# Kernel optimization log

Hardware: AMD Instinct MI355X
Metric: run time of the kernel (lower is better)

## Reference

```python
import jax, jax.numpy as jnp
import numpy as np

N_NODES = 50000
N_EDGES = 800000
IN_CH, HID_CH, OUT_CH = 256, 128, 64


def setup_inputs() -> dict:
    key = jax.random.key(0)
    k_x, k_e, k_w1, k_w2 = jax.random.split(key, 4)
    x = jax.random.normal(k_x, (N_NODES, IN_CH), dtype=jnp.float32)
    edge_index = jax.random.randint(k_e, (2, N_EDGES), 0, N_NODES, dtype=jnp.int32)
    # Glorot-style init like PyG GCNConv (weight [in, out], bias zeros)
    s1 = float(np.sqrt(6.0 / (IN_CH + HID_CH)))
    s2 = float(np.sqrt(6.0 / (HID_CH + OUT_CH)))
    W1 = jax.random.uniform(k_w1, (IN_CH, HID_CH), jnp.float32, -s1, s1)
    b1 = jnp.zeros((HID_CH,), jnp.float32)
    W2 = jax.random.uniform(k_w2, (HID_CH, OUT_CH), jnp.float32, -s2, s2)
    b2 = jnp.zeros((OUT_CH,), jnp.float32)
    return {"x": x, "edge_index": edge_index, "W1": W1, "b1": b1, "W2": W2, "b2": b2}


def _gcn_conv(x, src, dst, deg_inv_sqrt, W, b, n_nodes):
    """GCNConv with self-loops: D^{-1/2}(A+I)D^{-1/2} X W + b."""
    h = x @ W  # [N, out]
    norm = deg_inv_sqrt[src] * deg_inv_sqrt[dst]          # [E]
    msgs = h[src] * norm[:, None]                          # [E, out] gather
    agg = jax.ops.segment_sum(msgs, dst, num_segments=n_nodes)  # scatter-add
    self_loop = h * (deg_inv_sqrt * deg_inv_sqrt)[:, None]      # self-loop term
    return agg + self_loop + b


def reference(x, edge_index, W1, b1, W2, b2):
    n = x.shape[0]
    src, dst = edge_index[0], edge_index[1]
    # degree includes self-loop (+1), edge weight 1, counted at destination
    deg = jnp.zeros((n,), x.dtype).at[dst].add(1.0) + 1.0
    dis = jax.lax.rsqrt(deg)
    h = jax.nn.relu(_gcn_conv(x, src, dst, dis, W1, b1, n))
    out = jax.nn.relu(_gcn_conv(h, src, dst, dis, W2, b2, n))
    return out
```

## Files before the change

kernel.cpp:

```cpp
#include <hip/hip_runtime.h>

#define N_NODES 50000
#define N_EDGES 800000
#define IN_CH 256
#define HID_CH 128
#define OUT_CH 64
#define CAP 64
#define NBINS 196
#define PCHUNK 3200
#define PBLOCKS 250
#define SWZ_BLOCKS ((IN_CH * HID_CH + HID_CH * OUT_CH) / 256)

typedef _Float16 f16;
typedef _Float16 f16x8 __attribute__((ext_vector_type(8)));
typedef _Float16 f16x2 __attribute__((ext_vector_type(2)));
typedef float f32x4 __attribute__((ext_vector_type(4)));
typedef unsigned short u16;
typedef unsigned int u32;

__device__ __forceinline__ void local_scan(const int* __restrict__ binCnt,
                                           int* sc ,
                                           int* vout ) {
    int t = threadIdx.x & 255;
    int v = t < NBINS ? binCnt[t] : 0;
    sc[t] = v;
    vout[t] = v;
    __syncthreads();
#pragma unroll
    for (int ofs = 1; ofs < 256; ofs <<= 1) {
        int add = (t >= ofs) ? sc[t - ofs] : 0;
        __syncthreads();
        sc[t] += add;
        __syncthreads();
    }
}

template <int K, int N>
__device__ __forceinline__ void swz(const float* __restrict__ W, f16* __restrict__ Bsw,
                                    int idx) {
    constexpr int NTILES = N / 16;
    int j = idx & 7;
    int lane = (idx >> 3) & 63;
    int rest = idx >> 9;
    int nt = rest % NTILES;
    int ks = rest / NTILES;
    int k = ks * 32 + (lane >> 4) * 8 + j;
    int n = nt * 16 + (lane & 15);
    Bsw[idx] = (f16)W[(size_t)k * N + n];
}

__global__ __launch_bounds__(256) void k_pre(const int* __restrict__ dst,
                                             int* __restrict__ binCnt, int E,
                                             const float* __restrict__ W1,
                                             const float* __restrict__ W2,
                                             f16* __restrict__ B1,
                                             f16* __restrict__ B2) {
    if ((int)blockIdx.x < PBLOCKS) {
        __shared__ int lcnt[NBINS];
        for (int i = threadIdx.x; i < NBINS; i += 256) lcnt[i] = 0;
        __syncthreads();
        int base = blockIdx.x * PCHUNK;
        int end = min(base + PCHUNK, E);
        for (int i = base + (int)threadIdx.x; i < end; i += 256)
            atomicAdd(&lcnt[dst[i] >> 8], 1);
        __syncthreads();
        for (int i = threadIdx.x; i < NBINS; i += 256)
            if (lcnt[i]) atomicAdd(&binCnt[i], lcnt[i]);
        return;
    }
    int idx = ((int)blockIdx.x - PBLOCKS) * 256 + threadIdx.x;
    if (idx < IN_CH * HID_CH) {
        swz<IN_CH, HID_CH>(W1, B1, idx);
    } else {
        idx -= IN_CH * HID_CH;
        if (idx < HID_CH * OUT_CH) swz<HID_CH, OUT_CH>(W2, B2, idx);
    }
}

__global__ __launch_bounds__(256) void k_place(const int* __restrict__ src,
                                               const int* __restrict__ dst,
                                               const int* __restrict__ binCnt,
                                               int* __restrict__ binCursor,
                                               u32* __restrict__ ebuf, int E) {
    __shared__ u32 codes[PCHUNK];
    __shared__ int sc[256], vv[256];
    __shared__ int lcnt[NBINS], lbase[NBINS], lcur[NBINS];
    local_scan(binCnt, sc, vv);
    for (int i = threadIdx.x; i < NBINS; i += 256) lcnt[i] = 0;
    __syncthreads();
    int base = blockIdx.x * PCHUNK;
    int m = min(PCHUNK, E - base);
    for (int j = threadIdx.x; j < m; j += 256) {
        u32 d = (u32)dst[base + j];
        codes[j] = (d << 16) | (u32)src[base + j];
        atomicAdd(&lcnt[d >> 8], 1);
    }
    __syncthreads();
    for (int i = threadIdx.x; i < NBINS; i += 256) {
        lbase[i] = (sc[i] - vv[i]) + atomicAdd(&binCursor[i], lcnt[i]);
        lcur[i] = 0;
    }
    __syncthreads();
    for (int j = threadIdx.x; j < m; j += 256) {
        u32 c = codes[j];
        int b = c >> 24;
        int p = atomicAdd(&lcur[b], 1);
        ebuf[lbase[b] + p] = c;
    }
}

__global__ __launch_bounds__(256) void k_build(const u32* __restrict__ ebuf,
                                               const int* __restrict__ binCnt,
                                               int* __restrict__ cnt,
                                               float* __restrict__ dis,
                                               u16* __restrict__ bucket, int N) {
    __shared__ int sc[256], vv[256];
    __shared__ int lcnt[256];
    __shared__ u16 lbuck[256 * CAP];
    local_scan(binCnt, sc, vv);
    int t = threadIdx.x;
    lcnt[t] = 0;
    __syncthreads();
    int b = blockIdx.x;
    int s = sc[b] - vv[b];
    int e = sc[b];
    for (int i = s + t; i < e; i += 256) {
        u32 c = ebuf[i];
        int local = (c >> 16) & 255;
        int p = atomicAdd(&lcnt[local], 1);
        if (p < CAP) lbuck[local * CAP + p] = (u16)(c & 0xFFFFu);
    }
    __syncthreads();
    int nodeBase = b << 8;
    if (nodeBase + t < N) {
        cnt[nodeBase + t] = lcnt[t];
        dis[nodeBase + t] = rsqrtf((float)lcnt[t] + 1.0f);
    }
    const uint4* lsrc = (const uint4*)lbuck;
    uint4* gdst = (uint4*)(bucket + (size_t)nodeBase * CAP);
    for (int idx = t; idx < 256 * CAP / 8; idx += 256) {
        int row = idx >> 3;
        if (nodeBase + row < N) gdst[idx] = lsrc[idx];
    }
}

template <int K, int N, bool A_FP32, bool RELU>
__global__ __launch_bounds__(256) void k_gemm(const void* __restrict__ Av,
                                              const f16* __restrict__ Bsw,
                                              const float* __restrict__ dis,
                                              f16* __restrict__ C, int M) {
    constexpr int KSTEPS = K / 32, NTILES = N / 16;
    const int tid = threadIdx.x;
    const int wave = tid >> 6, lane = tid & 63;
    const int quad = lane >> 4, l16 = lane & 15;
    int row = blockIdx.x * 64 + wave * 16 + l16;
    const int rowc = row < M ? row : M - 1;

    f32x4 acc[NTILES];
#pragma unroll
    for (int t = 0; t < NTILES; ++t) acc[t] = (f32x4){0.f, 0.f, 0.f, 0.f};

#pragma unroll
    for (int ks = 0; ks < KSTEPS; ++ks) {
        f16x8 afrag;
        if (A_FP32) {
            const float* A = (const float*)Av;
            const float4* p = (const float4*)(A + (size_t)rowc * K + ks * 32 + quad * 8);
            float4 v0 = p[0], v1 = p[1];
            afrag[0] = (f16)v0.x; afrag[1] = (f16)v0.y;
            afrag[2] = (f16)v0.z; afrag[3] = (f16)v0.w;
            afrag[4] = (f16)v1.x; afrag[5] = (f16)v1.y;
            afrag[6] = (f16)v1.z; afrag[7] = (f16)v1.w;
        } else {
            const f16* A = (const f16*)Av;
            afrag = *(const f16x8*)(A + (size_t)rowc * K + ks * 32 + quad * 8);
            if (RELU) {
#pragma unroll
                for (int j = 0; j < 8; ++j)
                    afrag[j] = afrag[j] > (f16)0 ? afrag[j] : (f16)0;
            }
        }
#pragma unroll
        for (int t = 0; t < NTILES; ++t) {
            f16x8 bfrag = *(const f16x8*)(Bsw + (((size_t)ks * NTILES + t) * 64 + lane) * 8);
            acc[t] = __builtin_amdgcn_mfma_f32_16x16x32_f16(afrag, bfrag, acc[t], 0, 0, 0);
        }
    }

    int rbase = blockIdx.x * 64 + wave * 16 + quad * 4;
#pragma unroll
    for (int r = 0; r < 4; ++r) {
        int gr = rbase + r;
        if (gr < M) {
            float d = dis[gr];
#pragma unroll
            for (int t = 0; t < NTILES; ++t)
                C[(size_t)gr * N + t * 16 + l16] = (f16)(acc[t][r] * d);
        }
    }
}

#define APAD 136
__global__ __launch_bounds__(512) void k_pullgemm(const f16* __restrict__ g1,
                                                  const float* __restrict__ dis,
                                                  const float* __restrict__ b1,
                                                  const int* __restrict__ cnt,
                                                  const u16* __restrict__ bucket,
                                                  const f16* __restrict__ W2sw,
                                                  f16* __restrict__ g2, int N) {
    __shared__ f16 As[64][APAD];
    const int tid = threadIdx.x;
    const int wave = tid >> 6, lane = tid & 63;
    const int base = blockIdx.x * 64;

    float bv0 = b1[lane * 2], bv1 = b1[lane * 2 + 1];
    for (int i = 0; i < 8; ++i) {
        int uloc = wave * 8 + i;
        int u = base + uloc;
        if (u >= N) {
            f16x2 z; z[0] = (f16)0; z[1] = (f16)0;
            *(f16x2*)&As[uloc][lane * 2] = z;
            continue;
        }
        const f16* gp = g1 + lane * 2;
        f16x2 hv = *(const f16x2*)(gp + (size_t)u * HID_CH);
        float a0 = (float)hv[0], a1 = (float)hv[1];

        int n = cnt[u];
        if (n > CAP) n = CAP;
        const u16* row = bucket + u * CAP;
        int k = 0;
        for (; k + 8 <= n; k += 8) {
            uint4 iv = *(const uint4*)(row + k);
            int s0 = iv.x & 0xFFFF, s1 = iv.x >> 16;
            int s2 = iv.y & 0xFFFF, s3 = iv.y >> 16;
            int s4 = iv.z & 0xFFFF, s5 = iv.z >> 16;
            int s6 = iv.w & 0xFFFF, s7 = iv.w >> 16;
            f16x2 v0 = *(const f16x2*)(gp + (size_t)s0 * HID_CH);
            f16x2 v1 = *(const f16x2*)(gp + (size_t)s1 * HID_CH);
            f16x2 v2 = *(const f16x2*)(gp + (size_t)s2 * HID_CH);
            f16x2 v3 = *(const f16x2*)(gp + (size_t)s3 * HID_CH);
            f16x2 v4 = *(const f16x2*)(gp + (size_t)s4 * HID_CH);
            f16x2 v5 = *(const f16x2*)(gp + (size_t)s5 * HID_CH);
            f16x2 v6 = *(const f16x2*)(gp + (size_t)s6 * HID_CH);
            f16x2 v7 = *(const f16x2*)(gp + (size_t)s7 * HID_CH);
            a0 += ((float)v0[0] + (float)v1[0]) + ((float)v2[0] + (float)v3[0]) +
                  (((float)v4[0] + (float)v5[0]) + ((float)v6[0] + (float)v7[0]));
            a1 += ((float)v0[1] + (float)v1[1]) + ((float)v2[1] + (float)v3[1]) +
                  (((float)v4[1] + (float)v5[1]) + ((float)v6[1] + (float)v7[1]));
        }
        if (k + 4 <= n) {
            ushort4 s4v = *(const ushort4*)(row + k);
            f16x2 v0 = *(const f16x2*)(gp + (size_t)s4v.x * HID_CH);
            f16x2 v1 = *(const f16x2*)(gp + (size_t)s4v.y * HID_CH);
            f16x2 v2 = *(const f16x2*)(gp + (size_t)s4v.z * HID_CH);
            f16x2 v3 = *(const f16x2*)(gp + (size_t)s4v.w * HID_CH);
            a0 += ((float)v0[0] + (float)v1[0]) + ((float)v2[0] + (float)v3[0]);
            a1 += ((float)v0[1] + (float)v1[1]) + ((float)v2[1] + (float)v3[1]);
            k += 4;
        }
        for (; k < n; ++k) {
            f16x2 v = *(const f16x2*)(gp + (size_t)row[k] * HID_CH);
            a0 += (float)v[0];
            a1 += (float)v[1];
        }

        float du = dis[u];
        f16x2 o;
        o[0] = (f16)fmaxf(fmaf(du, a0, bv0), 0.f);
        o[1] = (f16)fmaxf(fmaf(du, a1, bv1), 0.f);
        *(f16x2*)&As[uloc][lane * 2] = o;
    }
    __syncthreads();

    constexpr int KSTEPS = HID_CH / 32;
    const int rg = wave >> 1;
    const int half = wave & 1;
    const int quad = lane >> 4, l16 = lane & 15;

    f32x4 acc[2];
    acc[0] = (f32x4){0.f, 0.f, 0.f, 0.f};
    acc[1] = (f32x4){0.f, 0.f, 0.f, 0.f};

#pragma unroll
    for (int ks = 0; ks < KSTEPS; ++ks) {
        f16x8 afrag = *(const f16x8*)&As[rg * 16 + l16][ks * 32 + quad * 8];
#pragma unroll
        for (int tt = 0; tt < 2; ++tt) {
            int nt = half * 2 + tt;
            f16x8 bfrag = *(const f16x8*)(W2sw + (((size_t)ks * 4 + nt) * 64 + lane) * 8);
            acc[tt] = __builtin_amdgcn_mfma_f32_16x16x32_f16(afrag, bfrag, acc[tt], 0, 0, 0);
        }
    }

    int rbase = base + rg * 16 + quad * 4;
#pragma unroll
    for (int r = 0; r < 4; ++r) {
        int gr = rbase + r;
        if (gr < N) {
            float d = dis[gr];
#pragma unroll
            for (int tt = 0; tt < 2; ++tt) {
                int nt = half * 2 + tt;
                g2[(size_t)gr * OUT_CH + nt * 16 + l16] = (f16)(acc[tt][r] * d);
            }
        }
    }
}

__global__ __launch_bounds__(256) void k_pull2(const f16* __restrict__ g,
                                               const float* __restrict__ dis,
                                               const float* __restrict__ bias,
                                               const int* __restrict__ cnt,
                                               const u16* __restrict__ bucket,
                                               float2* __restrict__ out, int N) {
    int tid = blockIdx.x * 256 + threadIdx.x;
    int u = tid >> 5;
    int sub = tid & 31;
    if (u >= N) return;
    const f16* gp = g + sub * 2;

    f16x2 hv = *(const f16x2*)(gp + (size_t)u * OUT_CH);
    float a0 = (float)hv[0], a1 = (float)hv[1];

    int n = cnt[u];
    if (n > CAP) n = CAP;
    const u16* row = bucket + u * CAP;

    int k = 0;
    for (; k + 8 <= n; k += 8) {
        uint4 iv = *(const uint4*)(row + k);
        int s0 = iv.x & 0xFFFF, s1 = iv.x >> 16;
        int s2 = iv.y & 0xFFFF, s3 = iv.y >> 16;
        int s4 = iv.z & 0xFFFF, s5 = iv.z >> 16;
        int s6 = iv.w & 0xFFFF, s7 = iv.w >> 16;
        f16x2 v0 = *(const f16x2*)(gp + (size_t)s0 * OUT_CH);
        f16x2 v1 = *(const f16x2*)(gp + (size_t)s1 * OUT_CH);
        f16x2 v2 = *(const f16x2*)(gp + (size_t)s2 * OUT_CH);
        f16x2 v3 = *(const f16x2*)(gp + (size_t)s3 * OUT_CH);
        f16x2 v4 = *(const f16x2*)(gp + (size_t)s4 * OUT_CH);
        f16x2 v5 = *(const f16x2*)(gp + (size_t)s5 * OUT_CH);
        f16x2 v6 = *(const f16x2*)(gp + (size_t)s6 * OUT_CH);
        f16x2 v7 = *(const f16x2*)(gp + (size_t)s7 * OUT_CH);
        a0 += ((float)v0[0] + (float)v1[0]) + ((float)v2[0] + (float)v3[0]) +
              (((float)v4[0] + (float)v5[0]) + ((float)v6[0] + (float)v7[0]));
        a1 += ((float)v0[1] + (float)v1[1]) + ((float)v2[1] + (float)v3[1]) +
              (((float)v4[1] + (float)v5[1]) + ((float)v6[1] + (float)v7[1]));
    }
    if (k + 4 <= n) {
        ushort4 s4v = *(const ushort4*)(row + k);
        f16x2 v0 = *(const f16x2*)(gp + (size_t)s4v.x * OUT_CH);
        f16x2 v1 = *(const f16x2*)(gp + (size_t)s4v.y * OUT_CH);
        f16x2 v2 = *(const f16x2*)(gp + (size_t)s4v.z * OUT_CH);
        f16x2 v3 = *(const f16x2*)(gp + (size_t)s4v.w * OUT_CH);
        a0 += ((float)v0[0] + (float)v1[0]) + ((float)v2[0] + (float)v3[0]);
        a1 += ((float)v0[1] + (float)v1[1]) + ((float)v2[1] + (float)v3[1]);
        k += 4;
    }
    for (; k < n; ++k) {
        f16x2 v = *(const f16x2*)(gp + (size_t)row[k] * OUT_CH);
        a0 += (float)v[0];
        a1 += (float)v[1];
    }

    float du = dis[u];
    float o0 = fmaf(du, a0, bias[sub * 2]);
    float o1 = fmaf(du, a1, bias[sub * 2 + 1]);
    out[(size_t)u * 32 + sub] = make_float2(fmaxf(o0, 0.f), fmaxf(o1, 0.f));
}


extern "C" void kernel_launch(void* const* d_in, const int* in_sizes, int n_in,
                              void* d_out, int out_size, void* d_ws, size_t ws_size,
                              hipStream_t stream) {
    const float* x  = (const float*)d_in[0];
    const int* ei   = (const int*)d_in[1];
    const float* W1 = (const float*)d_in[2];
    const float* b1 = (const float*)d_in[3];
    const float* W2 = (const float*)d_in[4];
    const float* b2 = (const float*)d_in[5];
    float* out = (float*)d_out;

    const int* src = ei;
    const int* dst = ei + N_EDGES;

    char* ws = (char*)d_ws;
    size_t off = 0;
    auto alloc = [&](size_t bytes) -> void* {
        off = (off + 255) & ~(size_t)255;
        void* p = ws + off;
        off += bytes;
        return p;
    };
    int*   binCnt    = (int*)alloc((size_t)NBINS * 2 * 4);
    int*   binCursor = binCnt + NBINS;
    u32*   ebuf      = (u32*)alloc((size_t)N_EDGES * 4);
    int*   cnt       = (int*)alloc((size_t)N_NODES * 4);
    float* dis       = (float*)alloc((size_t)N_NODES * 4);
    u16*   bucket    = (u16*)alloc((size_t)N_NODES * CAP * 2);
    f16*   W1sw      = (f16*)alloc((size_t)IN_CH * HID_CH * 2);
    f16*   W2sw      = (f16*)alloc((size_t)HID_CH * OUT_CH * 2);
    f16*   g1        = (f16*)alloc((size_t)N_NODES * HID_CH * 2);
    f16*   g2        = (f16*)alloc((size_t)N_NODES * OUT_CH * 2);

    hipMemsetAsync(binCnt, 0, (size_t)NBINS * 2 * 4, stream);

    k_pre<<<PBLOCKS + SWZ_BLOCKS, 256, 0, stream>>>(dst, binCnt, N_EDGES,
                                                    W1, W2, W1sw, W2sw);
    k_place<<<PBLOCKS, 256, 0, stream>>>(src, dst, binCnt, binCursor, ebuf, N_EDGES);
    k_build<<<NBINS, 256, 0, stream>>>(ebuf, binCnt, cnt, dis, bucket, N_NODES);

    k_gemm<IN_CH, HID_CH, true, false><<<(N_NODES + 63) / 64, 256, 0, stream>>>(
        x, W1sw, dis, g1, N_NODES);

    k_pullgemm<<<(N_NODES + 63) / 64, 512, 0, stream>>>(g1, dis, b1, cnt, bucket,
                                                        W2sw, g2, N_NODES);

    k_pull2<<<(N_NODES * 32 + 255) / 256, 256, 0, stream>>>(g2, dis, b2, cnt, bucket,
                                                            (float2*)out, N_NODES);
}
```

Baseline: 203.3 us.

## Fuse GCN pipeline into one cooperative persistent kernel with grid syncs

Replaces the six separate kernel launches with a single cooperative persistent kernel of 256 blocks x 512 threads. Grid-wide syncs separate the phases (histogram, place, build, gemm, pullgemm, pull2). The first GEMM no longer waits for degrees: the src-side dis scaling moves into the gather loops and is applied per neighbour, so GEMM1 can overlap with edge placement on a separate set of blocks, guarded by a flag spin-wait on the weight swizzle. The aim is to remove launch gaps and tail idle time. In exchange it adds grid-sync costs, an extra dis load per gathered edge, and lower occupancy from the fixed grid, with the old separate kernels kept as a fallback.

Result: slower. 642.9 us (+216.2%).

```diff
diff --git a/kernel.cpp b/kernel.cpp
--- a/kernel.cpp
+++ b/kernel.cpp
@@ -1,4 +1,7 @@
 #include <hip/hip_runtime.h>
+#include <hip/hip_cooperative_groups.h>
+
+namespace cg = cooperative_groups;
 
 #define N_NODES 50000
 #define N_EDGES 800000
@@ -7,33 +10,25 @@
 #define OUT_CH 64
 #define CAP 64
 #define NBINS 196
-#define PCHUNK 3200
-#define PBLOCKS 250
-#define SWZ_BLOCKS ((IN_CH * HID_CH + HID_CH * OUT_CH) / 256)
+#define NTHREADS 512
+#define NBLOCKS 256
+#define PBLOCKS 128
+#define PCHUNK 6250
+#define GB (NBLOCKS - PBLOCKS)
+#define SWZ_ELEMS (IN_CH * HID_CH + HID_CH * OUT_CH)
+#define SWZ_BLOCKS (SWZ_ELEMS / NTHREADS)
+#define G1_TILES ((N_NODES + 127) / 128)
+#define PG_TILES ((N_NODES + 63) / 64)
+#define APAD 136
 
 typedef _Float16 f16;
 typedef _Float16 f16x8 __attribute__((ext_vector_type(8)));
+typedef _Float16 f16x4v __attribute__((ext_vector_type(4)));
 typedef _Float16 f16x2 __attribute__((ext_vector_type(2)));
 typedef float f32x4 __attribute__((ext_vector_type(4)));
 typedef unsigned short u16;
 typedef unsigned int u32;
 
-__device__ __forceinline__ void local_scan(const int* __restrict__ binCnt,
-                                           int* sc ,
-                                           int* vout ) {
-    int t = threadIdx.x & 255;
-    int v = t < NBINS ? binCnt[t] : 0;
-    sc[t] = v;
-    vout[t] = v;
-    __syncthreads();
-#pragma unroll
-    for (int ofs = 1; ofs < 256; ofs <<= 1) {
-        int add = (t >= ofs) ? sc[t - ofs] : 0;
-        __syncthreads();
-        sc[t] += add;
-        __syncthreads();
-    }
-}
 
 template <int K, int N>
 __device__ __forceinline__ void swz(const float* __restrict__ W, f16* __restrict__ Bsw,
@@ -49,59 +44,65 @@
     Bsw[idx] = (f16)W[(size_t)k * N + n];
 }
 
-__global__ __launch_bounds__(256) void k_pre(const int* __restrict__ dst,
-                                             int* __restrict__ binCnt, int E,
-                                             const float* __restrict__ W1,
-                                             const float* __restrict__ W2,
-                                             f16* __restrict__ B1,
-                                             f16* __restrict__ B2) {
-    if ((int)blockIdx.x < PBLOCKS) {
-        __shared__ int lcnt[NBINS];
-        for (int i = threadIdx.x; i < NBINS; i += 256) lcnt[i] = 0;
+__device__ __forceinline__ void swz_all(int idx, const float* __restrict__ W1,
+                                        const float* __restrict__ W2,
+                                        f16* __restrict__ W1sw, f16* __restrict__ W2sw) {
+    if (idx < IN_CH * HID_CH) swz<IN_CH, HID_CH>(W1, W1sw, idx);
+    else if (idx < SWZ_ELEMS) swz<HID_CH, OUT_CH>(W2, W2sw, idx - IN_CH * HID_CH);
+}
+
+__device__ __forceinline__ void hist_chunk(int chunk, const int* __restrict__ dst,
+                                           int* __restrict__ binCnt, int* lcnt) {
+    const int tid = threadIdx.x;
+    for (int i = tid; i < NBINS; i += NTHREADS) lcnt[i] = 0;
+    __syncthreads();
+    int base = chunk * PCHUNK;
+    for (int i = tid; i < PCHUNK; i += NTHREADS)
+        atomicAdd(&lcnt[dst[base + i] >> 8], 1);
+    __syncthreads();
+    for (int i = tid; i < NBINS; i += NTHREADS)
+        if (lcnt[i]) atomicAdd(&binCnt[i], lcnt[i]);
+}
+
+__device__ __forceinline__ void scan_local(const int* __restrict__ binCnt,
+                                           int* sc, int* vv) {
+    const int t = threadIdx.x;
+    if (t < 256) {
+        int v = (t < NBINS) ? binCnt[t] : 0;
+        sc[t] = v; vv[t] = v;
+    }
+    __syncthreads();
+    for (int ofs = 1; ofs < 256; ofs <<= 1) {
+        int add = 0;
+        if (t < 256 && t >= ofs) add = sc[t - ofs];
         __syncthreads();
-        int base = blockIdx.x * PCHUNK;
-        int end = min(base + PCHUNK, E);
-        for (int i = base + (int)threadIdx.x; i < end; i += 256)
-            atomicAdd(&lcnt[dst[i] >> 8], 1);
+        if (t < 256) sc[t] += add;
         __syncthreads();
-        for (int i = threadIdx.x; i < NBINS; i += 256)
-            if (lcnt[i]) atomicAdd(&binCnt[i], lcnt[i]);
-        return;
-    }
-    int idx = ((int)blockIdx.x - PBLOCKS) * 256 + threadIdx.x;
-    if (idx < IN_CH * HID_CH) {
-        swz<IN_CH, HID_CH>(W1, B1, idx);
-    } else {
-        idx -= IN_CH * HID_CH;
-        if (idx < HID_CH * OUT_CH) swz<HID_CH, OUT_CH>(W2, B2, idx);
-    }
-}
-
-__global__ __launch_bounds__(256) void k_place(const int* __restrict__ src,
-                                               const int* __restrict__ dst,
-                                               const int* __restrict__ binCnt,
-                                               int* __restrict__ binCursor,
-                                               u32* __restrict__ ebuf, int E) {
-    __shared__ u32 codes[PCHUNK];
-    __shared__ int sc[256], vv[256];
-    __shared__ int lcnt[NBINS], lbase[NBINS], lcur[NBINS];
-    local_scan(binCnt, sc, vv);
-    for (int i = threadIdx.x; i < NBINS; i += 256) lcnt[i] = 0;
-    __syncthreads();
-    int base = blockIdx.x * PCHUNK;
-    int m = min(PCHUNK, E - base);
-    for (int j = threadIdx.x; j < m; j += 256) {
+    }
+}
+
+__device__ __forceinline__ void place_chunk(int chunk, const int* __restrict__ src,
+                                            const int* __restrict__ dst,
+                                            const int* sc, const int* vv,
+                                            int* __restrict__ binCursor,
+                                            u32* __restrict__ ebuf,
+                                            u32* codes, int* lcnt, int* lbase, int* lcur) {
+    const int tid = threadIdx.x;
+    for (int i = tid; i < NBINS; i += NTHREADS) lcnt[i] = 0;
+    __syncthreads();
+    int base = chunk * PCHUNK;
+    for (int j = tid; j < PCHUNK; j += NTHREADS) {
         u32 d = (u32)dst[base + j];
         codes[j] = (d << 16) | (u32)src[base + j];
         atomicAdd(&lcnt[d >> 8], 1);
     }
     __syncthreads();
-    for (int i = threadIdx.x; i < NBINS; i += 256) {
+    for (int i = tid; i < NBINS; i += NTHREADS) {
         lbase[i] = (sc[i] - vv[i]) + atomicAdd(&binCursor[i], lcnt[i]);
         lcur[i] = 0;
     }
     __syncthreads();
-    for (int j = threadIdx.x; j < m; j += 256) {
+    for (int j = tid; j < PCHUNK; j += NTHREADS) {
         u32 c = codes[j];
         int b = c >> 24;
         int p = atomicAdd(&lcur[b], 1);
@@ -109,22 +110,16 @@
     }
 }
 
-__global__ __launch_bounds__(256) void k_build(const u32* __restrict__ ebuf,
-                                               const int* __restrict__ binCnt,
-                                               int* __restrict__ cnt,
-                                               float* __restrict__ dis,
-                                               u16* __restrict__ bucket, int N) {
-    __shared__ int sc[256], vv[256];
-    __shared__ int lcnt[256];
-    __shared__ u16 lbuck[256 * CAP];
-    local_scan(binCnt, sc, vv);
-    int t = threadIdx.x;
-    lcnt[t] = 0;
-    __syncthreads();
-    int b = blockIdx.x;
-    int s = sc[b] - vv[b];
-    int e = sc[b];
-    for (int i = s + t; i < e; i += 256) {
+__device__ __forceinline__ void build_bin(int b, const u32* __restrict__ ebuf,
+                                          const int* sc, const int* vv,
+                                          int* __restrict__ cnt, float* __restrict__ dis,
+                                          u16* __restrict__ bucket,
+                                          int* lcnt, u16* lbuck) {
+    const int tid = threadIdx.x;
+    if (tid < 256) lcnt[tid] = 0;
+    __syncthreads();
+    int s = sc[b] - vv[b], e = sc[b];
+    for (int i = s + tid; i < e; i += NTHREADS) {
         u32 c = ebuf[i];
         int local = (c >> 16) & 255;
         int p = atomicAdd(&lcnt[local], 1);
@@ -132,99 +127,85 @@
     }
     __syncthreads();
     int nodeBase = b << 8;
-    if (nodeBase + t < N) {
-        cnt[nodeBase + t] = lcnt[t];
-        dis[nodeBase + t] = rsqrtf((float)lcnt[t] + 1.0f);
-    }
-    const uint4* lsrc = (const uint4*)lbuck;
-    uint4* gdst = (uint4*)(bucket + (size_t)nodeBase * CAP);
-    for (int idx = t; idx < 256 * CAP / 8; idx += 256) {
+    if (tid < 256 && nodeBase + tid < N_NODES) {
+        cnt[nodeBase + tid] = lcnt[tid];
+        dis[nodeBase + tid] = rsqrtf((float)lcnt[tid] + 1.0f);
+    }
+    const uint4* ls = (const uint4*)lbuck;
+    uint4* gd = (uint4*)(bucket + (size_t)nodeBase * CAP);
+    for (int idx = tid; idx < 256 * CAP / 8; idx += NTHREADS) {
         int row = idx >> 3;
-        if (nodeBase + row < N) gdst[idx] = lsrc[idx];
-    }
-}
-
-template <int K, int N, bool A_FP32, bool RELU>
-__global__ __launch_bounds__(256) void k_gemm(const void* __restrict__ Av,
-                                              const f16* __restrict__ Bsw,
-                                              const float* __restrict__ dis,
-                                              f16* __restrict__ C, int M) {
-    constexpr int KSTEPS = K / 32, NTILES = N / 16;
+        if (nodeBase + row < N_NODES) gd[idx] = ls[idx];
+    }
+}
+
+__device__ __forceinline__ void gemm1_tile(int t, const float* __restrict__ x,
+                                           const f16* __restrict__ W1sw,
+                                           f16* __restrict__ h1) {
     const int tid = threadIdx.x;
     const int wave = tid >> 6, lane = tid & 63;
     const int quad = lane >> 4, l16 = lane & 15;
-    int row = blockIdx.x * 64 + wave * 16 + l16;
-    const int rowc = row < M ? row : M - 1;
-
-    f32x4 acc[NTILES];
-#pragma unroll
-    for (int t = 0; t < NTILES; ++t) acc[t] = (f32x4){0.f, 0.f, 0.f, 0.f};
-
-#pragma unroll
-    for (int ks = 0; ks < KSTEPS; ++ks) {
+    int row = t * 128 + wave * 16 + l16;
+    const int rowc = row < N_NODES ? row : N_NODES - 1;
+
+    f32x4 acc[8];
+#pragma unroll
+    for (int n = 0; n < 8; ++n) acc[n] = (f32x4){0.f, 0.f, 0.f, 0.f};
+#pragma unroll
+    for (int ks = 0; ks < 8; ++ks) {
+        const float4* p = (const float4*)(x + (size_t)rowc * IN_CH + ks * 32 + quad * 8);
+        float4 v0 = p[0], v1 = p[1];
         f16x8 afrag;
-        if (A_FP32) {
-            const float* A = (const float*)Av;
-            const float4* p = (const float4*)(A + (size_t)rowc * K + ks * 32 + quad * 8);
-            float4 v0 = p[0], v1 = p[1];
-            afrag[0] = (f16)v0.x; afrag[1] = (f16)v0.y;
-            afrag[2] = (f16)v0.z; afrag[3] = (f16)v0.w;
-            afrag[4] = (f16)v1.x; afrag[5] = (f16)v1.y;
-            afrag[6] = (f16)v1.z; afrag[7] = (f16)v1.w;
-        } else {
-            const f16* A = (const f16*)Av;
-            afrag = *(const f16x8*)(A + (size_t)rowc * K + ks * 32 + quad * 8);
-            if (RELU) {
-#pragma unroll
-                for (int j = 0; j < 8; ++j)
-                    afrag[j] = afrag[j] > (f16)0 ? afrag[j] : (f16)0;
-            }
-        }
-#pragma unroll
-        for (int t = 0; t < NTILES; ++t) {
-            f16x8 bfrag = *(const f16x8*)(Bsw + (((size_t)ks * NTILES + t) * 64 + lane) * 8);
-            acc[t] = __builtin_amdgcn_mfma_f32_16x16x32_f16(afrag, bfrag, acc[t], 0, 0, 0);
-        }
-    }
-
-    int rbase = blockIdx.x * 64 + wave * 16 + quad * 4;
+        afrag[0] = (f16)v0.x; afrag[1] = (f16)v0.y;
+        afrag[2] = (f16)v0.z; afrag[3] = (f16)v0.w;
+        afrag[4] = (f16)v1.x; afrag[5] = (f16)v1.y;
+        afrag[6] = (f16)v1.z; afrag[7] = (f16)v1.w;
+#pragma unroll
+        for (int nt = 0; nt < 8; ++nt) {
+            f16x8 bfrag = *(const f16x8*)(W1sw + (((size_t)ks * 8 + nt) * 64 + lane) * 8);
+            acc[nt] = __builtin_amdgcn_mfma_f32_16x16x32_f16(afrag, bfrag, acc[nt], 0, 0, 0);
+        }
+    }
+    int rbase = t * 128 + wave * 16 + quad * 4;
 #pragma unroll
     for (int r = 0; r < 4; ++r) {
         int gr = rbase + r;
-        if (gr < M) {
-            float d = dis[gr];
-#pragma unroll
-            for (int t = 0; t < NTILES; ++t)
-                C[(size_t)gr * N + t * 16 + l16] = (f16)(acc[t][r] * d);
-        }
-    }
-}
-
-#define APAD 136
-__global__ __launch_bounds__(512) void k_pullgemm(const f16* __restrict__ g1,
-                                                  const float* __restrict__ dis,
-                                                  const float* __restrict__ b1,
-                                                  const int* __restrict__ cnt,
-                                                  const u16* __restrict__ bucket,
-                                                  const f16* __restrict__ W2sw,
-                                                  f16* __restrict__ g2, int N) {
-    __shared__ f16 As[64][APAD];
+        if (gr < N_NODES) {
+#pragma unroll
+            for (int nt = 0; nt < 8; ++nt)
+                h1[(size_t)gr * HID_CH + nt * 16 + l16] = (f16)acc[nt][r];
+        }
+    }
+}
+
+__device__ __forceinline__ void pullgemm_tile(int t, f16* AsRaw,
+                                              const f16* __restrict__ h1,
+                                              const float* __restrict__ dis,
+                                              const float* __restrict__ b1,
+                                              const int* __restrict__ cnt,
+                                              const u16* __restrict__ bucket,
+                                              const f16* __restrict__ W2sw,
+                                              f16* __restrict__ g2) {
+    typedef f16 (*As_t)[APAD];
+    As_t As = (As_t)AsRaw;
     const int tid = threadIdx.x;
     const int wave = tid >> 6, lane = tid & 63;
-    const int base = blockIdx.x * 64;
+    const int base = t * 64;
 
     float bv0 = b1[lane * 2], bv1 = b1[lane * 2 + 1];
     for (int i = 0; i < 8; ++i) {
         int uloc = wave * 8 + i;
         int u = base + uloc;
-        if (u >= N) {
+        if (u >= N_NODES) {
             f16x2 z; z[0] = (f16)0; z[1] = (f16)0;
             *(f16x2*)&As[uloc][lane * 2] = z;
             continue;
         }
-        const f16* gp = g1 + lane * 2;
+        float du = dis[u];
+        const f16* gp = h1 + lane * 2;
         f16x2 hv = *(const f16x2*)(gp + (size_t)u * HID_CH);
-        float a0 = (float)hv[0], a1 = (float)hv[1];
+        float a0 = du * (float)hv[0];
+        float a1 = du * (float)hv[1];
 
         int n = cnt[u];
         if (n > CAP) n = CAP;
@@ -236,6 +217,8 @@
             int s2 = iv.y & 0xFFFF, s3 = iv.y >> 16;
             int s4 = iv.z & 0xFFFF, s5 = iv.z >> 16;
             int s6 = iv.w & 0xFFFF, s7 = iv.w >> 16;
+            float d0 = dis[s0], d1 = dis[s1], d2 = dis[s2], d3 = dis[s3];
+            float d4 = dis[s4], d5 = dis[s5], d6 = dis[s6], d7 = dis[s7];
             f16x2 v0 = *(const f16x2*)(gp + (size_t)s0 * HID_CH);
             f16x2 v1 = *(const f16x2*)(gp + (size_t)s1 * HID_CH);
             f16x2 v2 = *(const f16x2*)(gp + (size_t)s2 * HID_CH);
@@ -244,28 +227,22 @@
             f16x2 v5 = *(const f16x2*)(gp + (size_t)s5 * HID_CH);
             f16x2 v6 = *(const f16x2*)(gp + (size_t)s6 * HID_CH);
             f16x2 v7 = *(const f16x2*)(gp + (size_t)s7 * HID_CH);
-            a0 += ((float)v0[0] + (float)v1[0]) + ((float)v2[0] + (float)v3[0]) +
-                  (((float)v4[0] + (float)v5[0]) + ((float)v6[0] + (float)v7[0]));
-            a1 += ((float)v0[1] + (float)v1[1]) + ((float)v2[1] + (float)v3[1]) +
-                  (((float)v4[1] + (float)v5[1]) + ((float)v6[1] + (float)v7[1]));
-        }
-        if (k + 4 <= n) {
-            ushort4 s4v = *(const ushort4*)(row + k);
-            f16x2 v0 = *(const f16x2*)(gp + (size_t)s4v.x * HID_CH);
-            f16x2 v1 = *(const f16x2*)(gp + (size_t)s4v.y * HID_CH);
-            f16x2 v2 = *(const f16x2*)(gp + (size_t)s4v.z * HID_CH);
-            f16x2 v3 = *(const f16x2*)(gp + (size_t)s4v.w * HID_CH);
-            a0 += ((float)v0[0] + (float)v1[0]) + ((float)v2[0] + (float)v3[0]);
-            a1 += ((float)v0[1] + (float)v1[1]) + ((float)v2[1] + (float)v3[1]);
-            k += 4;
+            a0 = fmaf(d0, (float)v0[0], a0); a1 = fmaf(d0, (float)v0[1], a1);
+            a0 = fmaf(d1, (float)v1[0], a0); a1 = fmaf(d1, (float)v1[1], a1);
+            a0 = fmaf(d2, (float)v2[0], a0); a1 = fmaf(d2, (float)v2[1], a1);
+            a0 = fmaf(d3, (float)v3[0], a0); a1 = fmaf(d3, (float)v3[1], a1);
+            a0 = fmaf(d4, (float)v4[0], a0); a1 = fmaf(d4, (float)v4[1], a1);
+            a0 = fmaf(d5, (float)v5[0], a0); a1 = fmaf(d5, (float)v5[1], a1);
+            a0 = fmaf(d6, (float)v6[0], a0); a1 = fmaf(d6, (float)v6[1], a1);
+            a0 = fmaf(d7, (float)v7[0], a0); a1 = fmaf(d7, (float)v7[1], a1);
         }
         for (; k < n; ++k) {
-            f16x2 v = *(const f16x2*)(gp + (size_t)row[k] * HID_CH);
-            a0 += (float)v[0];
-            a1 += (float)v[1];
-        }
-
-        float du = dis[u];
+            int s = row[k];
+            float d = dis[s];
+            f16x2 v = *(const f16x2*)(gp + (size_t)s * HID_CH);
+            a0 = fmaf(d, (float)v[0], a0);
+            a1 = fmaf(d, (float)v[1], a1);
+        }
         f16x2 o;
         o[0] = (f16)fmaxf(fmaf(du, a0, bv0), 0.f);
         o[1] = (f16)fmaxf(fmaf(du, a1, bv1), 0.f);
@@ -273,17 +250,13 @@
     }
     __syncthreads();
 
-    constexpr int KSTEPS = HID_CH / 32;
-    const int rg = wave >> 1;
-    const int half = wave & 1;
+    const int rg = wave >> 1, half = wave & 1;
     const int quad = lane >> 4, l16 = lane & 15;
-
     f32x4 acc[2];
     acc[0] = (f32x4){0.f, 0.f, 0.f, 0.f};
     acc[1] = (f32x4){0.f, 0.f, 0.f, 0.f};
-
-#pragma unroll
-    for (int ks = 0; ks < KSTEPS; ++ks) {
+#pragma unroll
+    for (int ks = 0; ks < 4; ++ks) {
         f16x8 afrag = *(const f16x8*)&As[rg * 16 + l16][ks * 32 + quad * 8];
 #pragma unroll
         for (int tt = 0; tt < 2; ++tt) {
@@ -292,12 +265,11 @@
             acc[tt] = __builtin_amdgcn_mfma_f32_16x16x32_f16(afrag, bfrag, acc[tt], 0, 0, 0);
         }
     }
-
     int rbase = base + rg * 16 + quad * 4;
 #pragma unroll
     for (int r = 0; r < 4; ++r) {
         int gr = rbase + r;
-        if (gr < N) {
+        if (gr < N_NODES) {
             float d = dis[gr];
 #pragma unroll
             for (int tt = 0; tt < 2; ++tt) {
@@ -306,27 +278,22 @@
             }
         }
     }
-}
-
-__global__ __launch_bounds__(256) void k_pull2(const f16* __restrict__ g,
-                                               const float* __restrict__ dis,
-                                               const float* __restrict__ bias,
-                                               const int* __restrict__ cnt,
-                                               const u16* __restrict__ bucket,
-                                               float2* __restrict__ out, int N) {
-    int tid = blockIdx.x * 256 + threadIdx.x;
-    int u = tid >> 5;
-    int sub = tid & 31;
-    if (u >= N) return;
-    const f16* gp = g + sub * 2;
-
-    f16x2 hv = *(const f16x2*)(gp + (size_t)u * OUT_CH);
+    __syncthreads();
+}
+
+__device__ __forceinline__ void pull2_node(int u, int sub, const f16* __restrict__ g2,
+                                           const float* __restrict__ dis,
+                                           const float* __restrict__ b2,
+                                           const int* __restrict__ cnt,
+                                           const u16* __restrict__ bucket,
+                                           float4* __restrict__ out) {
+    const f16* gp = g2 + sub * 4;
+    f16x4v hv = *(const f16x4v*)(gp + (size_t)u * OUT_CH);
     float a0 = (float)hv[0], a1 = (float)hv[1];
-
+    float a2 = (float)hv[2], a3 = (float)hv[3];
     int n = cnt[u];
     if (n > CAP) n = CAP;
     const u16* row = bucket + u * CAP;
-
     int k = 0;
     for (; k + 8 <= n; k += 8) {
         uint4 iv = *(const uint4*)(row + k);
@@ -334,39 +301,183 @@
         int s2 = iv.y & 0xFFFF, s3 = iv.y >> 16;
         int s4 = iv.z & 0xFFFF, s5 = iv.z >> 16;
         int s6 = iv.w & 0xFFFF, s7 = iv.w >> 16;
-        f16x2 v0 = *(const f16x2*)(gp + (size_t)s0 * OUT_CH);
-        f16x2 v1 = *(const f16x2*)(gp + (size_t)s1 * OUT_CH);
-        f16x2 v2 = *(const f16x2*)(gp + (size_t)s2 * OUT_CH);
-        f16x2 v3 = *(const f16x2*)(gp + (size_t)s3 * OUT_CH);
-        f16x2 v4 = *(const f16x2*)(gp + (size_t)s4 * OUT_CH);
-        f16x2 v5 = *(const f16x2*)(gp + (size_t)s5 * OUT_CH);
-        f16x2 v6 = *(const f16x2*)(gp + (size_t)s6 * OUT_CH);
-        f16x2 v7 = *(const f16x2*)(gp + (size_t)s7 * OUT_CH);
+        f16x4v v0 = *(const f16x4v*)(gp + (size_t)s0 * OUT_CH);
+        f16x4v v1 = *(const f16x4v*)(gp + (size_t)s1 * OUT_CH);
+        f16x4v v2 = *(const f16x4v*)(gp + (size_t)s2 * OUT_CH);
+        f16x4v v3 = *(const f16x4v*)(gp + (size_t)s3 * OUT_CH);
+        f16x4v v4 = *(const f16x4v*)(gp + (size_t)s4 * OUT_CH);
+        f16x4v v5 = *(const f16x4v*)(gp + (size_t)s5 * OUT_CH);
+        f16x4v v6 = *(const f16x4v*)(gp + (size_t)s6 * OUT_CH);
+        f16x4v v7 = *(const f16x4v*)(gp + (size_t)s7 * OUT_CH);
         a0 += ((float)v0[0] + (float)v1[0]) + ((float)v2[0] + (float)v3[0]) +
               (((float)v4[0] + (float)v5[0]) + ((float)v6[0] + (float)v7[0]));
         a1 += ((float)v0[1] + (float)v1[1]) + ((float)v2[1] + (float)v3[1]) +
               (((float)v4[1] + (float)v5[1]) + ((float)v6[1] + (float)v7[1]));
-    }
-    if (k + 4 <= n) {
-        ushort4 s4v = *(const ushort4*)(row + k);
-        f16x2 v0 = *(const f16x2*)(gp + (size_t)s4v.x * OUT_CH);
-        f16x2 v1 = *(const f16x2*)(gp + (size_t)s4v.y * OUT_CH);
-        f16x2 v2 = *(const f16x2*)(gp + (size_t)s4v.z * OUT_CH);
-        f16x2 v3 = *(const f16x2*)(gp + (size_t)s4v.w * OUT_CH);
-        a0 += ((float)v0[0] + (float)v1[0]) + ((float)v2[0] + (float)v3[0]);
-        a1 += ((float)v0[1] + (float)v1[1]) + ((float)v2[1] + (float)v3[1]);
-        k += 4;
+        a2 += ((float)v0[2] + (float)v1[2]) + ((float)v2[2] + (float)v3[2]) +
+              (((float)v4[2] + (float)v5[2]) + ((float)v6[2] + (float)v7[2]));
+        a3 += ((float)v0[3] + (float)v1[3]) + ((float)v2[3] + (float)v3[3]) +
+              (((float)v4[3] + (float)v5[3]) + ((float)v6[3] + (float)v7[3]));
     }
     for (; k < n; ++k) {
-        f16x2 v = *(const f16x2*)(gp + (size_t)row[k] * OUT_CH);
-        a0 += (float)v[0];
-        a1 += (float)v[1];
-    }
-
+        f16x4v v = *(const f16x4v*)(gp + (size_t)row[k] * OUT_CH);
+        a0 += (float)v[0]; a1 += (float)v[1];
+        a2 += (float)v[2]; a3 += (float)v[3];
+    }
     float du = dis[u];
-    float o0 = fmaf(du, a0, bias[sub * 2]);
-    float o1 = fmaf(du, a1, bias[sub * 2 + 1]);
-    out[(size_t)u * 32 + sub] = make_float2(fmaxf(o0, 0.f), fmaxf(o1, 0.f));
+    float4 o;
+    o.x = fmaxf(fmaf(du, a0, b2[sub * 4]), 0.f);
+    o.y = fmaxf(fmaf(du, a1, b2[sub * 4 + 1]), 0.f);
+    o.z = fmaxf(fmaf(du, a2, b2[sub * 4 + 2]), 0.f);
+    o.w = fmaxf(fmaf(du, a3, b2[sub * 4 + 3]), 0.f);
+    out[(size_t)u * 16 + sub] = o;
+}
+
+__global__ __launch_bounds__(NTHREADS, 2) void k_mega(
+    const float* __restrict__ x, const int* __restrict__ src, const int* __restrict__ dst,
+    const float* __restrict__ W1, const float* __restrict__ b1,
+    const float* __restrict__ W2, const float* __restrict__ b2,
+    int* __restrict__ binCnt, int* __restrict__ binCursor, int* __restrict__ flags,
+    u32* __restrict__ ebuf, int* __restrict__ cnt, float* __restrict__ dis,
+    u16* __restrict__ bucket, f16* __restrict__ W1sw, f16* __restrict__ W2sw,
+    f16* __restrict__ h1, f16* __restrict__ g2, float4* __restrict__ out) {
+    __shared__ __align__(16) char smem[37888];
+    int* z0 = (int*)smem;
+    int* sc = (int*)(smem + 1024);
+    int* vv = (int*)(smem + 2048);
+    int* z1 = (int*)(smem + 3072);
+    int* z2 = (int*)(smem + 4096);
+    char* payload = smem + 5120;
+
+    const int bid = blockIdx.x;
+    const int tid = threadIdx.x;
+    cg::grid_group grid = cg::this_grid();
+
+    if (bid < PBLOCKS) {
+        hist_chunk(bid, dst, binCnt, z0);
+        __threadfence();
+        __syncthreads();
+        if (tid == 0) {
+            atomicAdd(&flags[0], 1);
+            while (atomicAdd(&flags[0], 0) < PBLOCKS) __builtin_amdgcn_s_sleep(2);
+        }
+        __syncthreads();
+        __threadfence();
+        scan_local(binCnt, sc, vv);
+        place_chunk(bid, src, dst, sc, vv, binCursor, ebuf,
+                    (u32*)payload, z0, z1, z2);
+    } else {
+        const int sb = bid - PBLOCKS;
+        if (sb < SWZ_BLOCKS) {
+            swz_all(sb * NTHREADS + tid, W1, W2, W1sw, W2sw);
+            __threadfence();
+            __syncthreads();
+            if (tid == 0) atomicAdd(&flags[2], 1);
+        }
+        if (tid == 0)
+            while (atomicAdd(&flags[2], 0) < SWZ_BLOCKS) __builtin_amdgcn_s_sleep(2);
+        __syncthreads();
+        __threadfence();
+        for (int t = sb; t < G1_TILES; t += GB)
+            gemm1_tile(t, x, W1sw, h1);
+    }
+
+    __threadfence();
+    grid.sync();
+
+    scan_local(binCnt, sc, vv);
+    if (bid < NBINS)
+        build_bin(bid, ebuf, sc, vv, cnt, dis, bucket, z0, (u16*)payload);
+
+    __threadfence();
+    grid.sync();
+
+    for (int t = bid; t < PG_TILES; t += NBLOCKS)
+        pullgemm_tile(t, (f16*)payload, h1, dis, b1, cnt, bucket, W2sw, g2);
+
+    __threadfence();
+    grid.sync();
+
+    {
+        const int gtid = bid * NTHREADS + tid;
+        const int sub = gtid & 15;
+        const int ustep = (NBLOCKS * NTHREADS) / 16;
+        for (int ubase = 0; ubase < N_NODES; ubase += ustep) {
+            int u = ubase + (gtid >> 4);
+            if (u < N_NODES) pull2_node(u, sub, g2, dis, b2, cnt, bucket, out);
+        }
+    }
+}
+
+
+__global__ __launch_bounds__(NTHREADS) void k_pre_sb(const int* __restrict__ dst,
+                                                     int* __restrict__ binCnt,
+                                                     const float* __restrict__ W1,
+                                                     const float* __restrict__ W2,
+                                                     f16* __restrict__ W1sw,
+                                                     f16* __restrict__ W2sw) {
+    if ((int)blockIdx.x < PBLOCKS) {
+        __shared__ int lcnt[256];
+        hist_chunk(blockIdx.x, dst, binCnt, lcnt);
+    } else {
+        swz_all(((int)blockIdx.x - PBLOCKS) * NTHREADS + threadIdx.x, W1, W2, W1sw, W2sw);
+    }
+}
+
+__global__ __launch_bounds__(NTHREADS) void k_place_sb(const int* __restrict__ src,
+                                                       const int* __restrict__ dst,
+                                                       const int* __restrict__ binCnt,
+                                                       int* __restrict__ binCursor,
+                                                       u32* __restrict__ ebuf) {
+    __shared__ __align__(16) char smem[5120 + PCHUNK * 4];
+    int* z0 = (int*)smem;
+    int* sc = (int*)(smem + 1024);
+    int* vv = (int*)(smem + 2048);
+    int* z1 = (int*)(smem + 3072);
+    int* z2 = (int*)(smem + 4096);
+    scan_local(binCnt, sc, vv);
+    place_chunk(blockIdx.x, src, dst, sc, vv, binCursor, ebuf,
+                (u32*)(smem + 5120), z0, z1, z2);
+}
+
+__global__ __launch_bounds__(NTHREADS) void k_build_sb(const u32* __restrict__ ebuf,
+                                                       const int* __restrict__ binCnt,
+                                                       int* __restrict__ cnt,
+                                                       float* __restrict__ dis,
+                                                       u16* __restrict__ bucket) {
+    __shared__ __align__(16) char smem[3072 + 256 * CAP * 2];
+    int* z0 = (int*)smem;
+    int* sc = (int*)(smem + 1024);
+    int* vv = (int*)(smem + 2048);
+    scan_local(binCnt, sc, vv);
+    build_bin(blockIdx.x, ebuf, sc, vv, cnt, dis, bucket, z0, (u16*)(smem + 3072));
+}
+
+__global__ __launch_bounds__(NTHREADS) void k_gemm1_sb(const float* __restrict__ x,
+                                                       const f16* __restrict__ W1sw,
+                                                       f16* __restrict__ h1) {
+    gemm1_tile(blockIdx.x, x, W1sw, h1);
+}
+
+__global__ __launch_bounds__(NTHREADS) void k_pullgemm_sb(const f16* __restrict__ h1,
+                                                          const float* __restrict__ dis,
+                                                          const float* __restrict__ b1,
+                                                          const int* __restrict__ cnt,
+                                                          const u16* __restrict__ bucket,
+                                                          const f16* __restrict__ W2sw,
+                                                          f16* __restrict__ g2) {
+    __shared__ __align__(16) f16 As[64 * APAD];
+    pullgemm_tile(blockIdx.x, As, h1, dis, b1, cnt, bucket, W2sw, g2);
+}
+
+__global__ __launch_bounds__(NTHREADS) void k_pull2_sb(const f16* __restrict__ g2,
+                                                       const float* __restrict__ dis,
+                                                       const float* __restrict__ b2,
+                                                       const int* __restrict__ cnt,
+                                                       const u16* __restrict__ bucket,
+                                                       float4* __restrict__ out) {
+    int gtid = blockIdx.x * NTHREADS + threadIdx.x;
+    int u = gtid >> 4;
+    if (u < N_NODES) pull2_node(u, gtid & 15, g2, dis, b2, cnt, bucket, out);
 }
 
 
@@ -379,7 +490,7 @@
     const float* b1 = (const float*)d_in[3];
     const float* W2 = (const float*)d_in[4];
     const float* b2 = (const float*)d_in[5];
-    float* out = (float*)d_out;
+    float4* out = (float4*)d_out;
 
     const int* src = ei;
     const int* dst = ei + N_EDGES;
@@ -392,30 +503,36 @@
         off += bytes;
         return p;
     };
-    int*   binCnt    = (int*)alloc((size_t)NBINS * 2 * 4);
-    int*   binCursor = binCnt + NBINS;
-    u32*   ebuf      = (u32*)alloc((size_t)N_EDGES * 4);
-    int*   cnt       = (int*)alloc((size_t)N_NODES * 4);
-    float* dis       = (float*)alloc((size_t)N_NODES * 4);
-    u16*   bucket    = (u16*)alloc((size_t)N_NODES * CAP * 2);
-    f16*   W1sw      = (f16*)alloc((size_t)IN_CH * HID_CH * 2);
-    f16*   W2sw      = (f16*)alloc((size_t)HID_CH * OUT_CH * 2);
-    f16*   g1        = (f16*)alloc((size_t)N_NODES * HID_CH * 2);
-    f16*   g2        = (f16*)alloc((size_t)N_NODES * OUT_CH * 2);
-
-    hipMemsetAsync(binCnt, 0, (size_t)NBINS * 2 * 4, stream);
-
-    k_pre<<<PBLOCKS + SWZ_BLOCKS, 256, 0, stream>>>(dst, binCnt, N_EDGES,
-                                                    W1, W2, W1sw, W2sw);
-    k_place<<<PBLOCKS, 256, 0, stream>>>(src, dst, binCnt, binCursor, ebuf, N_EDGES);
-    k_build<<<NBINS, 256, 0, stream>>>(ebuf, binCnt, cnt, dis, bucket, N_NODES);
-
-    k_gemm<IN_CH, HID_CH, true, false><<<(N_NODES + 63) / 64, 256, 0, stream>>>(
-        x, W1sw, dis, g1, N_NODES);
-
-    k_pullgemm<<<(N_NODES + 63) / 64, 512, 0, stream>>>(g1, dis, b1, cnt, bucket,
-                                                        W2sw, g2, N_NODES);
-
-    k_pull2<<<(N_NODES * 32 + 255) / 256, 256, 0, stream>>>(g2, dis, b2, cnt, bucket,
-                                                            (float2*)out, N_NODES);
-}
+    int*   zbuf   = (int*)alloc((size_t)(NBINS * 2 + 8) * 4);
+    int*   binCnt = zbuf;
+    int*   binCursor = zbuf + NBINS;
+    int*   flags  = zbuf + 2 * NBINS;
+    u32*   ebuf   = (u32*)alloc((size_t)N_EDGES * 4);
+    int*   cnt    = (int*)alloc((size_t)N_NODES * 4);
+    float* dis    = (float*)alloc((size_t)N_NODES * 4);
+    u16*   bucket = (u16*)alloc((size_t)N_NODES * CAP * 2);
+    f16*   W1sw   = (f16*)alloc((size_t)IN_CH * HID_CH * 2);
+    f16*   W2sw   = (f16*)alloc((size_t)HID_CH * OUT_CH * 2);
+    f16*   h1     = (f16*)alloc((size_t)N_NODES * HID_CH * 2);
+    f16*   g2     = (f16*)alloc((size_t)N_NODES * OUT_CH * 2);
+
+    hipMemsetAsync(zbuf, 0, (size_t)(NBINS * 2 + 8) * 4, stream);
+
+    void* args[] = {
+        (void*)&x, (void*)&src, (void*)&dst, (void*)&W1, (void*)&b1,
+        (void*)&W2, (void*)&b2, (void*)&binCnt, (void*)&binCursor, (void*)&flags,
+        (void*)&ebuf, (void*)&cnt, (void*)&dis, (void*)&bucket, (void*)&W1sw,
+        (void*)&W2sw, (void*)&h1, (void*)&g2, (void*)&out
+    };
+    hipError_t err = hipLaunchCooperativeKernel((const void*)k_mega, dim3(NBLOCKS),
+                                                dim3(NTHREADS), args, 0, stream);
+    if (err != hipSuccess) {
+        k_pre_sb<<<PBLOCKS + SWZ_BLOCKS, NTHREADS, 0, stream>>>(dst, binCnt, W1, W2, W1sw, W2sw);
+        k_place_sb<<<PBLOCKS, NTHREADS, 0, stream>>>(src, dst, binCnt, binCursor, ebuf);
+        k_build_sb<<<NBINS, NTHREADS, 0, stream>>>(ebuf, binCnt, cnt, dis, bucket);
+        k_gemm1_sb<<<G1_TILES, NTHREADS, 0, stream>>>(x, W1sw, h1);
+        k_pullgemm_sb<<<PG_TILES, NTHREADS, 0, stream>>>(h1, dis, b1, cnt, bucket, W2sw, g2);
+        k_pull2_sb<<<(N_NODES * 16 + NTHREADS - 1) / NTHREADS, NTHREADS, 0, stream>>>(
+            g2, dis, b2, cnt, bucket, out);
+    }
+}
```
